# Kernel tuning notes

Hardware: AMD Instinct MI355X
Metric: run time of the kernel (lower is better)

The kernel has to match this reference:

```python
import jax, jax.numpy as jnp
import numpy as np

B, H, S, D = 2, 16, 2048, 64
MASK_NEG = 1e9


def setup_inputs() -> dict:
    key = jax.random.key(0)
    kq, kk, kv, km = jax.random.split(key, 4)
    Q = jax.random.normal(kq, (B, H, S, D), dtype=jnp.float32)
    K = jax.random.normal(kk, (B, H, S, D), dtype=jnp.float32)
    V = jax.random.normal(kv, (B, H, S, D), dtype=jnp.float32)
    # float 0/1 mask, broadcast over heads; 1 = masked-out position
    attn_mask = jax.random.randint(km, (B, 1, S, S), 0, 2).astype(jnp.float32)
    return {"Q": Q, "K": K, "V": V, "attn_mask": attn_mask}


def reference(Q, K, V, attn_mask):
    # scores: [B, H, S, S]
    attn_score = jnp.einsum('bhqd,bhkd->bhqk', Q, K)
    scale = jnp.sqrt(jnp.asarray(K.shape[-1], dtype=jnp.float32))
    attn_scale = attn_score / scale - MASK_NEG * attn_mask
    attn_prob = jax.nn.softmax(attn_scale, axis=-1)
    attn_out = jnp.einsum('bhqk,bhkd->bhqd', attn_prob, V)
    return attn_out
```

## Files before the change

kernel.cpp:

```cpp
#include <hip/hip_runtime.h>


#define S_LEN 2048
#define D_DIM 64
#define WPR   32
#define NIT   32

typedef __attribute__((ext_vector_type(8)))  short bf16x8;
typedef __attribute__((ext_vector_type(4)))  float f32x4;
typedef __attribute__((ext_vector_type(16))) float f32x16;
typedef unsigned long long ull;

__device__ __forceinline__ f32x16 mfma32(bf16x8 a, bf16x8 b, f32x16 c) {
  return __builtin_amdgcn_mfma_f32_32x32x16_bf16(a, b, c, 0, 0, 0);
}
__device__ __forceinline__ f32x4 mfma16(bf16x8 a, bf16x8 b, f32x4 c) {
  return __builtin_amdgcn_mfma_f32_16x16x32_bf16(a, b, c, 0, 0, 0);
}
__device__ __forceinline__ unsigned short f2bf(float f) {
  unsigned u = __builtin_bit_cast(unsigned, f);
  unsigned r = u + 0x7FFFu + ((u >> 16) & 1u);
  return (unsigned short)(r >> 16);
}
__device__ __forceinline__ float bf2f(unsigned short s) {
  unsigned u = ((unsigned)s) << 16;
  return __builtin_bit_cast(float, u);
}
__device__ __forceinline__ unsigned packbf(float a, float b) {
#if __has_builtin(__builtin_amdgcn_cvt_pk_bf16_f32)
  typedef __bf16 bfv2 __attribute__((ext_vector_type(2)));
  bfv2 v = __builtin_amdgcn_cvt_pk_bf16_f32(a, b);
  return __builtin_bit_cast(unsigned, v);
#else
  unsigned ua = __builtin_bit_cast(unsigned, a);
  unsigned ub = __builtin_bit_cast(unsigned, b);
  ua = ua + 0x7FFFu + ((ua >> 16) & 1u);
  ub = ub + 0x7FFFu + ((ub >> 16) & 1u);
  return (ua >> 16) | (ub & 0xFFFF0000u);
#endif
}
__device__ __forceinline__ float fexp2(float x) {
#if __has_builtin(__builtin_amdgcn_exp2f)
  return __builtin_amdgcn_exp2f(x);
#else
  return exp2f(x);
#endif
}
__device__ __forceinline__ bool detect_bf16(const void* maskp) {
  const unsigned short* s = (const unsigned short*)maskp;
  unsigned short v = s[2 * (threadIdx.x & 63)];
  return __ballot(v == (unsigned short)0x3F80) != 0ull;
}
__device__ __forceinline__ int4 cvt_f8(const float* p) {
  float4 f0 = *(const float4*)p;
  float4 f1 = *(const float4*)(p + 4);
  int4 r;
  r.x = (int)packbf(f0.x, f0.y);
  r.y = (int)packbf(f0.z, f0.w);
  r.z = (int)packbf(f1.x, f1.y);
  r.w = (int)packbf(f1.z, f1.w);
  return r;
}

#define C1 0.18033688011112042f
#define C2 1.4426950408889634e9f

__global__ __launch_bounds__(256) void prep_all(
    const void* __restrict__ M, const void* __restrict__ Kin,
    const void* __restrict__ Vin, const void* __restrict__ Qin,
    ull* __restrict__ bits, unsigned short* __restrict__ Kf,
    unsigned short* __restrict__ Vf, unsigned short* __restrict__ Qc) {
  __shared__ __align__(16) unsigned short T[64 * 72];
  const bool isb = detect_bf16(M);
  const unsigned bx = blockIdx.x;
  const int tid = threadIdx.x;

  if (bx < 32768u) {
    unsigned idx = bx * 256u + tid;
    bool on = isb ? (bf2f(((const unsigned short*)M)[idx]) > 0.5f)
                  : (((const float*)M)[idx] > 0.5f);
    ull bm = __ballot(on);
    if ((tid & 63) == 0) {
      unsigned c = idx & 2047u, r = (idx >> 11) & 2047u, bb = idx >> 22;
      bits[(((size_t)(bb * WPR + (c >> 6))) << 11) + r] = bm;
    }
  } else if (bx < 32768u + 2048u) {
    unsigned g = (bx - 32768u) * 256u + tid;
    unsigned lane = g & 63u, f = (g >> 6) & 7u, it = (g >> 9) & 31u, bh = g >> 14;
    unsigned t = f >> 2, dc = f & 3, hi = lane >> 5, l31 = lane & 31;
    size_t src = (size_t)bh * (S_LEN * D_DIM) +
                 (size_t)(it * 64 + t * 32 + l31) * D_DIM + dc * 16 + hi * 8;
    int4 out;
    if (isb) out = *(const int4*)((const unsigned short*)Kin + src);
    else     out = cvt_f8((const float*)Kin + src);
    *(int4*)&Kf[(size_t)g * 8] = out;
  } else if (bx < 32768u + 2048u + 1024u) {
    unsigned idx = bx - (32768u + 2048u);
    unsigned bh = idx >> 5, it = idx & 31u;
    {
      int k = tid >> 2, d0 = (tid & 3) * 16;
      size_t src = (size_t)bh * (S_LEN * D_DIM) + (size_t)(it * 64 + k) * D_DIM + d0;
      int4 a, c;
      if (isb) {
        const unsigned short* s = (const unsigned short*)Vin + src;
        a = *(const int4*)s; c = *(const int4*)(s + 8);
      } else {
        const float* s = (const float*)Vin + src;
        a = cvt_f8(s); c = cvt_f8(s + 8);
      }
      *(int4*)&T[k * 72 + d0] = a;
      *(int4*)&T[k * 72 + d0 + 8] = c;
    }
    __syncthreads();
    #pragma unroll
    for (int h = 0; h < 2; ++h) {
      int c = tid + h * 256;
      int lane = c & 63, f = c >> 6;
      int t = f >> 2, kc = (f >> 1) & 1, dt = f & 1;
      int hi = lane >> 5, l31 = lane & 31;
      unsigned short v[8];
      #pragma unroll
      for (int j = 0; j < 8; ++j)
        v[j] = T[(t * 32 + kc * 16 + hi * 8 + j) * 72 + dt * 32 + l31];
      *(int4*)&Vf[(((size_t)(bh * 32 + it)) * 8 + f) * 512 + lane * 8] = *(int4*)v;
    }
  } else {
    size_t i0 = ((size_t)(bx - (32768u + 2048u + 1024u)) * 256 + tid) * 8;
    unsigned short v[8];
    if (isb) {
      *(int4*)v = *(const int4*)((const unsigned short*)Qin + i0);
      #pragma unroll
      for (int j = 0; j < 8; ++j) v[j] = f2bf(bf2f(v[j]) * C1);
    } else {
      const float* f = (const float*)Qin + i0;
      #pragma unroll
      for (int j = 0; j < 4; ++j)
        *((unsigned*)v + j) = packbf(f[2 * j] * C1, f[2 * j + 1] * C1);
    }
    *(int4*)&Qc[i0] = *(int4*)v;
  }
}

__global__ __launch_bounds__(256, 4) void attn_fast(
    const unsigned short* __restrict__ Qc, const unsigned short* __restrict__ Kf,
    const unsigned short* __restrict__ Vf, const ull* __restrict__ bits,
    const void* __restrict__ maskp, void* __restrict__ Op) {
  __shared__ float Comb[2][32][64];
  __shared__ float Lc[4][32];

  const bool isb = detect_bf16(maskp);
  const int tid  = threadIdx.x;
  const int wave = tid >> 6;
  const int lane = tid & 63;
  const int hi   = lane >> 5;
  const int l31  = lane & 31;
  const int id   = blockIdx.x;
  const int slot = id >> 3;
  const int bh   = (id & 7) * 4 + (slot & 3);
  const int q0   = (slot >> 2) * 32;
  const int b    = bh >> 4;
  const size_t base = (size_t)bh * S_LEN * D_DIM;
  const int xidx = ((lane ^ 32) & 63) * 4;

  bf16x8 qf[4];
  #pragma unroll
  for (int dc = 0; dc < 4; ++dc)
    qf[dc] = *(const bf16x8*)&Qc[base + (size_t)(q0 + l31) * D_DIM + dc * 16 + hi * 8];

  f32x16 acc_o[2];
  float lsum = 0.f;
  #pragma unroll
  for (int r = 0; r < 16; ++r) { acc_o[0][r] = 0.f; acc_o[1][r] = 0.f; }

  for (int i = 0; i < NIT / 4; ++i) {
    const int it = wave * (NIT / 4) + i;
    const size_t fb = ((size_t)(bh * 32 + it)) * 8 * 512;

    ull w = bits[(((size_t)(b * WPR + it)) << 11) + q0 + l31] >> (hi * 4);
    unsigned wt[2] = {(unsigned)w, (unsigned)(w >> 32)};

    #pragma unroll
    for (int t = 0; t < 2; ++t) {
      const unsigned short* Kb = Kf + fb + (size_t)(t * 4) * 512 + lane * 8;
      f32x16 sc;
      #pragma unroll
      for (int r = 0; r < 16; ++r) sc[r] = 0.f;
      #pragma unroll
      for (int dc = 0; dc < 4; ++dc) {
        bf16x8 kfr = *(const bf16x8*)(Kb + dc * 512);
        sc = mfma32(kfr, qf[dc], sc);
      }

      float p[16];
      #pragma unroll
      for (int r = 0; r < 16; ++r) {
        float e = fexp2(sc[r]);
        unsigned bit = (wt[t] >> ((r & 3) + 8 * (r >> 2))) & 1u;
        p[r] = bit ? 0.0f : e;
        lsum += p[r];
      }

      #pragma unroll
      for (int kc = 0; kc < 2; ++kc) {
        unsigned pk0 = packbf(p[8 * kc + 0], p[8 * kc + 1]);
        unsigned pk1 = packbf(p[8 * kc + 2], p[8 * kc + 3]);
        unsigned pk2 = packbf(p[8 * kc + 4], p[8 * kc + 5]);
        unsigned pk3 = packbf(p[8 * kc + 6], p[8 * kc + 7]);
        unsigned x0 = (unsigned)__builtin_amdgcn_ds_bpermute(xidx, (int)pk0);
        unsigned x1 = (unsigned)__builtin_amdgcn_ds_bpermute(xidx, (int)pk1);
        unsigned x2 = (unsigned)__builtin_amdgcn_ds_bpermute(xidx, (int)pk2);
        unsigned x3 = (unsigned)__builtin_amdgcn_ds_bpermute(xidx, (int)pk3);
        uint4 d;
        d.x = hi ? x2 : pk0;
        d.y = hi ? x3 : pk1;
        d.z = hi ? pk2 : x0;
        d.w = hi ? pk3 : x1;
        bf16x8 pf = __builtin_bit_cast(bf16x8, d);

        const unsigned short* Vb = Vf + fb + (size_t)(t * 4 + kc * 2) * 512 + lane * 8;
        #pragma unroll
        for (int dt = 0; dt < 2; ++dt) {
          bf16x8 vfr = *(const bf16x8*)(Vb + dt * 512);
          acc_o[dt] = mfma32(pf, vfr, acc_o[dt]);
        }
      }
    }
  }

  {
    int li = __builtin_bit_cast(int, lsum);
    float other = __builtin_bit_cast(float, __builtin_amdgcn_ds_bpermute(xidx, li));
    lsum += other;
  }

  __syncthreads();
  if (wave >= 2) {
    #pragma unroll
    for (int dt = 0; dt < 2; ++dt)
      #pragma unroll
      for (int r = 0; r < 16; ++r)
        Comb[wave - 2][dt * 16 + r][lane] = acc_o[dt][r];
  }
  if (hi == 0) Lc[wave][l31] = lsum;
  __syncthreads();
  if (wave < 2) {
    #pragma unroll
    for (int dt = 0; dt < 2; ++dt)
      #pragma unroll
      for (int r = 0; r < 16; ++r)
        acc_o[dt][r] += Comb[wave][dt * 16 + r][lane];
  }
  __syncthreads();
  if (wave == 1) {
    #pragma unroll
    for (int dt = 0; dt < 2; ++dt)
      #pragma unroll
      for (int r = 0; r < 16; ++r)
        Comb[0][dt * 16 + r][lane] = acc_o[dt][r];
  }
  __syncthreads();
  if (wave == 0) {
    #pragma unroll
    for (int r = 0; r < 16; ++r) {
      int m = (r & 3) + 8 * (r >> 2) + 4 * hi;
      float o0 = acc_o[0][r] + Comb[0][r][lane];
      float o1 = acc_o[1][r] + Comb[0][16 + r][lane];
      float lv = Lc[0][m] + Lc[1][m] + Lc[2][m] + Lc[3][m];
      float inv = 1.0f / lv;
      size_t idx = base + (size_t)(q0 + m) * D_DIM + l31;
      if (isb) {
        ((unsigned short*)Op)[idx]      = f2bf(o0 * inv);
        ((unsigned short*)Op)[idx + 32] = f2bf(o1 * inv);
      } else {
        ((float*)Op)[idx]      = o0 * inv;
        ((float*)Op)[idx + 32] = o1 * inv;
      }
    }
  }
}

__global__ __launch_bounds__(256, 2) void attn_fallback(
    const void* __restrict__ Qp, const void* __restrict__ Kp,
    const void* __restrict__ Vp, const void* __restrict__ maskp,
    void* __restrict__ Op) {
  __shared__ __align__(16) short QKlds[128 * 72];
  __shared__ __align__(16) short Vtlds[64 * 72];
  __shared__ __align__(16) short Plds2[128 * 72];

  const bool isb = detect_bf16(maskp);
  const int tid  = threadIdx.x;
  const int wave = tid >> 6;
  const int lane = tid & 63;
  const int l15  = lane & 15;
  const int quad = lane >> 4;
  const int q0   = blockIdx.x * 128;
  const int bh   = blockIdx.y;
  const int b    = bh >> 4;
  const size_t base = (size_t)bh * S_LEN * D_DIM;

  const short* Qs = (const short*)Qp; const float* Qf = (const float*)Qp;
  const short* Ks = (const short*)Kp; const float* Kf2 = (const float*)Kp;
  const short* Vs = (const short*)Vp; const float* Vf2 = (const float*)Vp;

  if (isb) {
    const short* Qg = Qs + base + (size_t)q0 * D_DIM;
    #pragma unroll
    for (int p = 0; p < 4; ++p) {
      int e = p * 2048 + tid * 8;
      *(int4*)&QKlds[(e >> 6) * 72 + (e & 63)] = *(const int4*)(Qg + e);
    }
  } else {
    const float* Qg = Qf + base + (size_t)q0 * D_DIM;
    #pragma unroll
    for (int p = 0; p < 4; ++p) {
      int e = p * 2048 + tid * 8;
      *(int4*)&QKlds[(e >> 6) * 72 + (e & 63)] = cvt_f8(Qg + e);
    }
  }
  __syncthreads();
  bf16x8 qf[2][2];
  #pragma unroll
  for (int mi = 0; mi < 2; ++mi)
    #pragma unroll
    for (int kt = 0; kt < 2; ++kt)
      qf[mi][kt] = *(const bf16x8*)&QKlds[(wave * 32 + mi * 16 + l15) * 72 + kt * 32 + quad * 8];
  __syncthreads();

  f32x4 acc_o[2][4];
  f32x4 acc_l[2];
  const f32x4 zero4 = {0.f, 0.f, 0.f, 0.f};
  #pragma unroll
  for (int mi = 0; mi < 2; ++mi) {
    acc_l[mi] = zero4;
    #pragma unroll
    for (int nt = 0; nt < 4; ++nt) acc_o[mi][nt] = zero4;
  }
  bf16x8 onesB;
  {
    short ov = (l15 == 0) ? (short)0x3F80 : (short)0;
    #pragma unroll
    for (int i = 0; i < 8; ++i) onesB[i] = ov;
  }

  for (int it = 0; it < NIT; ++it) {
    const int k0 = it * 64;
    if (isb) {
      const short* Kg = Ks + base + (size_t)k0 * D_DIM;
      #pragma unroll
      for (int p = 0; p < 2; ++p) {
        int e = p * 2048 + tid * 8;
        *(int4*)&QKlds[(e >> 6) * 72 + (e & 63)] = *(const int4*)(Kg + e);
      }
    } else {
      const float* Kg = Kf2 + base + (size_t)k0 * D_DIM;
      #pragma unroll
      for (int p = 0; p < 2; ++p) {
        int e = p * 2048 + tid * 8;
        *(int4*)&QKlds[(e >> 6) * 72 + (e & 63)] = cvt_f8(Kg + e);
      }
    }
    {
      const int r0 = (tid >> 3) * 2;
      const int d0 = (tid & 7) * 8;
      unsigned short as_[8], bs_[8];
      if (isb) {
        const short* Vg = Vs + base + (size_t)k0 * D_DIM;
        *(int4*)as_ = *(const int4*)(Vg + r0 * D_DIM + d0);
        *(int4*)bs_ = *(const int4*)(Vg + (r0 + 1) * D_DIM + d0);
      } else {
        const float* Vg = Vf2 + base + (size_t)k0 * D_DIM;
        *(int4*)as_ = cvt_f8(Vg + r0 * D_DIM + d0);
        *(int4*)bs_ = cvt_f8(Vg + (r0 + 1) * D_DIM + d0);
      }
      #pragma unroll
      for (int j = 0; j < 8; ++j) {
        int d = d0 + j;
        int blk = (r0 >> 3) ^ (d >> 3);
        unsigned pk = (unsigned)as_[j] | ((unsigned)bs_[j] << 16);
        *(unsigned*)&Vtlds[d * 72 + blk * 8 + (r0 & 7)] = pk;
      }
    }
    __syncthreads();

    f32x4 sc[2][4];
    #pragma unroll
    for (int mi = 0; mi < 2; ++mi)
      #pragma unroll
      for (int nt = 0; nt < 4; ++nt) sc[mi][nt] = zero4;
    #pragma unroll
    for (int nt = 0; nt < 4; ++nt) {
      bf16x8 kf0 = *(const bf16x8*)&QKlds[(nt * 16 + l15) * 72 + quad * 8];
      bf16x8 kf1 = *(const bf16x8*)&QKlds[(nt * 16 + l15) * 72 + 32 + quad * 8];
      #pragma unroll
      for (int mi = 0; mi < 2; ++mi) {
        sc[mi][nt] = mfma16(qf[mi][0], kf0, sc[mi][nt]);
        sc[mi][nt] = mfma16(qf[mi][1], kf1, sc[mi][nt]);
      }
    }

    #pragma unroll
    for (int mi = 0; mi < 2; ++mi) {
      #pragma unroll
      for (int nt = 0; nt < 4; ++nt) {
        #pragma unroll
        for (int reg = 0; reg < 4; ++reg) {
          int rg = q0 + wave * 32 + mi * 16 + quad * 4 + reg;
          size_t mix = (size_t)b * S_LEN * S_LEN + (size_t)rg * S_LEN + k0 + nt * 16 + l15;
          float mv = isb ? bf2f(((const unsigned short*)maskp)[mix])
                         : ((const float*)maskp)[mix];
          float y = sc[mi][nt][reg] * C1 - mv * C2;
          Plds2[(wave * 32 + mi * 16 + quad * 4 + reg) * 72 + nt * 16 + l15] =
              (short)f2bf(fexp2(y));
        }
      }
    }
    __syncthreads();

    #pragma unroll
    for (int kt = 0; kt < 2; ++kt) {
      bf16x8 pf[2];
      #pragma unroll
      for (int mi = 0; mi < 2; ++mi)
        pf[mi] = *(const bf16x8*)&Plds2[(wave * 32 + mi * 16 + l15) * 72 + kt * 32 + quad * 8];
      #pragma unroll
      for (int nt = 0; nt < 4; ++nt) {
        int d = nt * 16 + l15;
        int kb = (kt * 4 + quad) ^ (d >> 3);
        bf16x8 vf = *(const bf16x8*)&Vtlds[d * 72 + kb * 8];
        #pragma unroll
        for (int mi = 0; mi < 2; ++mi)
          acc_o[mi][nt] = mfma16(pf[mi], vf, acc_o[mi][nt]);
      }
      #pragma unroll
      for (int mi = 0; mi < 2; ++mi)
        acc_l[mi] = mfma16(pf[mi], onesB, acc_l[mi]);
    }
    __syncthreads();
  }

  #pragma unroll
  for (int mi = 0; mi < 2; ++mi) {
    #pragma unroll
    for (int reg = 0; reg < 4; ++reg) {
      float lv = __shfl(acc_l[mi][reg], lane & 48, 64);
      float inv = 1.0f / lv;
      #pragma unroll
      for (int nt = 0; nt < 4; ++nt) {
        float o = acc_o[mi][nt][reg] * inv;
        size_t idx = base + (size_t)(q0 + wave * 32 + mi * 16 + quad * 4 + reg) * D_DIM + nt * 16 + l15;
        if (isb) ((unsigned short*)Op)[idx] = f2bf(o);
        else     ((float*)Op)[idx] = o;
      }
    }
  }
}

extern "C" void kernel_launch(void* const* d_in, const int* in_sizes, int n_in,
                              void* d_out, int out_size, void* d_ws, size_t ws_size,
                              hipStream_t stream) {
  const void* Q = d_in[0];
  const void* K = d_in[1];
  const void* V = d_in[2];
  const void* M = d_in[3];

  dim3 block(256);
  const size_t bits_bytes = (size_t)2 * S_LEN * S_LEN / 8;
  const size_t tens_bytes = (size_t)2 * 16 * S_LEN * D_DIM * 2;

  if (ws_size >= bits_bytes + 3 * tens_bytes) {
    char* ws = (char*)d_ws;
    ull* bits = (ull*)ws;
    unsigned short* Kf = (unsigned short*)(ws + bits_bytes);
    unsigned short* Vf = (unsigned short*)(ws + bits_bytes + tens_bytes);
    unsigned short* Qc = (unsigned short*)(ws + bits_bytes + 2 * tens_bytes);
    prep_all<<<dim3(32768 + 2048 + 1024 + 2048), block, 0, stream>>>(
        M, K, V, Q, bits, Kf, Vf, Qc);
    attn_fast<<<dim3(2048), block, 0, stream>>>(Qc, Kf, Vf, bits, M, d_out);
  } else {
    attn_fallback<<<dim3(S_LEN / 128, 32), block, 0, stream>>>(Q, K, V, M, d_out);
  }
}
```

Measured before the change: 187.1 us.

## Permute K rows and mask bits to drop P-fragment lane swaps; row sums via MFMA

The K fragment rows and the mask bitmask are permuted in the prep kernel, so the score MFMA output layout matches the A-operand layout of the PV MFMA. This removes the four ds_bpermute cross-lane swaps per P fragment. The row-sum accumulation is moved from scalar adds to an extra MFMA against a ones vector, with a new store pattern for the partial sums. The cost is one extra MFMA per PV step, 16 more accumulator registers and more complex index bookkeeping.

```diff
diff --git a/kernel.cpp b/kernel.cpp
--- a/kernel.cpp
+++ b/kernel.cpp
@@ -26,17 +26,14 @@
   unsigned u = ((unsigned)s) << 16;
   return __builtin_bit_cast(float, u);
 }
+typedef __bf16 bfv2 __attribute__((ext_vector_type(2)));
 __device__ __forceinline__ unsigned packbf(float a, float b) {
 #if __has_builtin(__builtin_amdgcn_cvt_pk_bf16_f32)
-  typedef __bf16 bfv2 __attribute__((ext_vector_type(2)));
   bfv2 v = __builtin_amdgcn_cvt_pk_bf16_f32(a, b);
   return __builtin_bit_cast(unsigned, v);
 #else
-  unsigned ua = __builtin_bit_cast(unsigned, a);
-  unsigned ub = __builtin_bit_cast(unsigned, b);
-  ua = ua + 0x7FFFu + ((ua >> 16) & 1u);
-  ub = ub + 0x7FFFu + ((ub >> 16) & 1u);
-  return (ua >> 16) | (ub & 0xFFFF0000u);
+  bfv2 v = {(__bf16)a, (__bf16)b};
+  return __builtin_bit_cast(unsigned, v);
 #endif
 }
 __device__ __forceinline__ float fexp2(float x) {
@@ -65,6 +62,11 @@
 #define C1 0.18033688011112042f
 #define C2 1.4426950408889634e9f
 
+__device__ __forceinline__ unsigned permrow(unsigned x) {
+  unsigned m12 = x & 12u;
+  return (m12 == 4u) ? x + 4u : (m12 == 8u) ? x - 4u : x;
+}
+
 __global__ __launch_bounds__(256) void prep_all(
     const void* __restrict__ M, const void* __restrict__ Kin,
     const void* __restrict__ Vin, const void* __restrict__ Qin,
@@ -81,6 +83,8 @@
                   : (((const float*)M)[idx] > 0.5f);
     ull bm = __ballot(on);
     if ((tid & 63) == 0) {
+      const ull M1 = 0x00F000F000F000F0ULL, M2 = 0x0F000F000F000F00ULL;
+      bm = (bm & ~(M1 | M2)) | ((bm & M1) << 4) | ((bm & M2) >> 4);
       unsigned c = idx & 2047u, r = (idx >> 11) & 2047u, bb = idx >> 22;
       bits[(((size_t)(bb * WPR + (c >> 6))) << 11) + r] = bm;
     }
@@ -89,7 +93,7 @@
     unsigned lane = g & 63u, f = (g >> 6) & 7u, it = (g >> 9) & 31u, bh = g >> 14;
     unsigned t = f >> 2, dc = f & 3, hi = lane >> 5, l31 = lane & 31;
     size_t src = (size_t)bh * (S_LEN * D_DIM) +
-                 (size_t)(it * 64 + t * 32 + l31) * D_DIM + dc * 16 + hi * 8;
+                 (size_t)(it * 64 + t * 32 + permrow(l31)) * D_DIM + dc * 16 + hi * 8;
     int4 out;
     if (isb) out = *(const int4*)((const unsigned short*)Kin + src);
     else     out = cvt_f8((const float*)Kin + src);
@@ -160,7 +164,6 @@
   const int q0   = (slot >> 2) * 32;
   const int b    = bh >> 4;
   const size_t base = (size_t)bh * S_LEN * D_DIM;
-  const int xidx = ((lane ^ 32) & 63) * 4;
 
   bf16x8 qf[4];
   #pragma unroll
@@ -168,9 +171,16 @@
     qf[dc] = *(const bf16x8*)&Qc[base + (size_t)(q0 + l31) * D_DIM + dc * 16 + hi * 8];
 
   f32x16 acc_o[2];
-  float lsum = 0.f;
+  f32x16 acc_l;
   #pragma unroll
-  for (int r = 0; r < 16; ++r) { acc_o[0][r] = 0.f; acc_o[1][r] = 0.f; }
+  for (int r = 0; r < 16; ++r) { acc_o[0][r] = 0.f; acc_o[1][r] = 0.f; acc_l[r] = 0.f; }
+
+  bf16x8 onesB;
+  {
+    short ov = (l31 == 0) ? (short)0x3F80 : (short)0;
+    #pragma unroll
+    for (int i = 0; i < 8; ++i) onesB[i] = ov;
+  }
 
   for (int i = 0; i < NIT / 4; ++i) {
     const int it = wave * (NIT / 4) + i;
@@ -197,24 +207,15 @@
         float e = fexp2(sc[r]);
         unsigned bit = (wt[t] >> ((r & 3) + 8 * (r >> 2))) & 1u;
         p[r] = bit ? 0.0f : e;
-        lsum += p[r];
       }
 
       #pragma unroll
       for (int kc = 0; kc < 2; ++kc) {
-        unsigned pk0 = packbf(p[8 * kc + 0], p[8 * kc + 1]);
-        unsigned pk1 = packbf(p[8 * kc + 2], p[8 * kc + 3]);
-        unsigned pk2 = packbf(p[8 * kc + 4], p[8 * kc + 5]);
-        unsigned pk3 = packbf(p[8 * kc + 6], p[8 * kc + 7]);
-        unsigned x0 = (unsigned)__builtin_amdgcn_ds_bpermute(xidx, (int)pk0);
-        unsigned x1 = (unsigned)__builtin_amdgcn_ds_bpermute(xidx, (int)pk1);
-        unsigned x2 = (unsigned)__builtin_amdgcn_ds_bpermute(xidx, (int)pk2);
-        unsigned x3 = (unsigned)__builtin_amdgcn_ds_bpermute(xidx, (int)pk3);
         uint4 d;
-        d.x = hi ? x2 : pk0;
-        d.y = hi ? x3 : pk1;
-        d.z = hi ? pk2 : x0;
-        d.w = hi ? pk3 : x1;
+        d.x = packbf(p[8 * kc + 0], p[8 * kc + 1]);
+        d.y = packbf(p[8 * kc + 2], p[8 * kc + 3]);
+        d.z = packbf(p[8 * kc + 4], p[8 * kc + 5]);
+        d.w = packbf(p[8 * kc + 6], p[8 * kc + 7]);
         bf16x8 pf = __builtin_bit_cast(bf16x8, d);
 
         const unsigned short* Vb = Vf + fb + (size_t)(t * 4 + kc * 2) * 512 + lane * 8;
@@ -223,14 +224,9 @@
           bf16x8 vfr = *(const bf16x8*)(Vb + dt * 512);
           acc_o[dt] = mfma32(pf, vfr, acc_o[dt]);
         }
-      }
-    }
-  }
-
-  {
-    int li = __builtin_bit_cast(int, lsum);
-    float other = __builtin_bit_cast(float, __builtin_amdgcn_ds_bpermute(xidx, li));
-    lsum += other;
+        acc_l = mfma32(pf, onesB, acc_l);
+      }
+    }
   }
 
   __syncthreads();
@@ -241,7 +237,11 @@
       for (int r = 0; r < 16; ++r)
         Comb[wave - 2][dt * 16 + r][lane] = acc_o[dt][r];
   }
-  if (hi == 0) Lc[wave][l31] = lsum;
+  if (l31 == 0) {
+    #pragma unroll
+    for (int r = 0; r < 16; ++r)
+      Lc[wave][(r & 3) + 8 * (r >> 2) + 4 * hi] = acc_l[r];
+  }
   __syncthreads();
   if (wave < 2) {
     #pragma unroll
```

Measured after the change: 194.0 us. 1.04x slower.

## Permute K rows and mask bits to drop bpermute exchange; prefetch K/V fragments

Applied to the files above, without the earlier changes.

The prep kernel now permutes K rows within each 32-row tile (swapping row groups 4-7 and 8-11) and applies the matching nibble swap to the packed mask bits. With that layout the P fragment produced by the QK^T MFMA can feed the PV MFMA directly, so the four ds_bpermute exchanges and selects per chunk are removed. The main loop also loads all K and V fragments for an iteration up front, before the mask word and the compute, to hide global load latency. This uses more registers and relies on the row permutation matching the MFMA output layout exactly.

```diff
diff --git a/kernel.cpp b/kernel.cpp
--- a/kernel.cpp
+++ b/kernel.cpp
@@ -65,6 +65,11 @@
 #define C1 0.18033688011112042f
 #define C2 1.4426950408889634e9f
 
+__device__ __forceinline__ unsigned permrow(unsigned x) {
+  unsigned m12 = x & 12u;
+  return (m12 == 4u) ? x + 4u : (m12 == 8u) ? x - 4u : x;
+}
+
 __global__ __launch_bounds__(256) void prep_all(
     const void* __restrict__ M, const void* __restrict__ Kin,
     const void* __restrict__ Vin, const void* __restrict__ Qin,
@@ -81,6 +86,8 @@
                   : (((const float*)M)[idx] > 0.5f);
     ull bm = __ballot(on);
     if ((tid & 63) == 0) {
+      const ull M1 = 0x00F000F000F000F0ULL, M2 = 0x0F000F000F000F00ULL;
+      bm = (bm & ~(M1 | M2)) | ((bm & M1) << 4) | ((bm & M2) >> 4);
       unsigned c = idx & 2047u, r = (idx >> 11) & 2047u, bb = idx >> 22;
       bits[(((size_t)(bb * WPR + (c >> 6))) << 11) + r] = bm;
     }
@@ -89,7 +96,7 @@
     unsigned lane = g & 63u, f = (g >> 6) & 7u, it = (g >> 9) & 31u, bh = g >> 14;
     unsigned t = f >> 2, dc = f & 3, hi = lane >> 5, l31 = lane & 31;
     size_t src = (size_t)bh * (S_LEN * D_DIM) +
-                 (size_t)(it * 64 + t * 32 + l31) * D_DIM + dc * 16 + hi * 8;
+                 (size_t)(it * 64 + t * 32 + permrow(l31)) * D_DIM + dc * 16 + hi * 8;
     int4 out;
     if (isb) out = *(const int4*)((const unsigned short*)Kin + src);
     else     out = cvt_f8((const float*)Kin + src);
@@ -175,21 +182,31 @@
   for (int i = 0; i < NIT / 4; ++i) {
     const int it = wave * (NIT / 4) + i;
     const size_t fb = ((size_t)(bh * 32 + it)) * 8 * 512;
-
+    const unsigned short* Fb = Kf + fb + lane * 8;
+    const unsigned short* Vb = Vf + fb + lane * 8;
+
+    bf16x8 kfr[2][4], vfr[2][4];
+    #pragma unroll
+    for (int t = 0; t < 2; ++t)
+      #pragma unroll
+      for (int dc = 0; dc < 4; ++dc)
+        kfr[t][dc] = *(const bf16x8*)(Fb + (size_t)(t * 4 + dc) * 512);
+    #pragma unroll
+    for (int t = 0; t < 2; ++t)
+      #pragma unroll
+      for (int f = 0; f < 4; ++f)
+        vfr[t][f] = *(const bf16x8*)(Vb + (size_t)(t * 4 + f) * 512);
     ull w = bits[(((size_t)(b * WPR + it)) << 11) + q0 + l31] >> (hi * 4);
     unsigned wt[2] = {(unsigned)w, (unsigned)(w >> 32)};
 
     #pragma unroll
     for (int t = 0; t < 2; ++t) {
-      const unsigned short* Kb = Kf + fb + (size_t)(t * 4) * 512 + lane * 8;
       f32x16 sc;
       #pragma unroll
       for (int r = 0; r < 16; ++r) sc[r] = 0.f;
       #pragma unroll
-      for (int dc = 0; dc < 4; ++dc) {
-        bf16x8 kfr = *(const bf16x8*)(Kb + dc * 512);
-        sc = mfma32(kfr, qf[dc], sc);
-      }
+      for (int dc = 0; dc < 4; ++dc)
+        sc = mfma32(kfr[t][dc], qf[dc], sc);
 
       float p[16];
       #pragma unroll
@@ -202,27 +219,15 @@
 
       #pragma unroll
       for (int kc = 0; kc < 2; ++kc) {
-        unsigned pk0 = packbf(p[8 * kc + 0], p[8 * kc + 1]);
-        unsigned pk1 = packbf(p[8 * kc + 2], p[8 * kc + 3]);
-        unsigned pk2 = packbf(p[8 * kc + 4], p[8 * kc + 5]);
-        unsigned pk3 = packbf(p[8 * kc + 6], p[8 * kc + 7]);
-        unsigned x0 = (unsigned)__builtin_amdgcn_ds_bpermute(xidx, (int)pk0);
-        unsigned x1 = (unsigned)__builtin_amdgcn_ds_bpermute(xidx, (int)pk1);
-        unsigned x2 = (unsigned)__builtin_amdgcn_ds_bpermute(xidx, (int)pk2);
-        unsigned x3 = (unsigned)__builtin_amdgcn_ds_bpermute(xidx, (int)pk3);
         uint4 d;
-        d.x = hi ? x2 : pk0;
-        d.y = hi ? x3 : pk1;
-        d.z = hi ? pk2 : x0;
-        d.w = hi ? pk3 : x1;
+        d.x = packbf(p[8 * kc + 0], p[8 * kc + 1]);
+        d.y = packbf(p[8 * kc + 2], p[8 * kc + 3]);
+        d.z = packbf(p[8 * kc + 4], p[8 * kc + 5]);
+        d.w = packbf(p[8 * kc + 6], p[8 * kc + 7]);
         bf16x8 pf = __builtin_bit_cast(bf16x8, d);
-
-        const unsigned short* Vb = Vf + fb + (size_t)(t * 4 + kc * 2) * 512 + lane * 8;
         #pragma unroll
-        for (int dt = 0; dt < 2; ++dt) {
-          bf16x8 vfr = *(const bf16x8*)(Vb + dt * 512);
-          acc_o[dt] = mfma32(pf, vfr, acc_o[dt]);
-        }
+        for (int dt = 0; dt < 2; ++dt)
+          acc_o[dt] = mfma32(pf, vfr[t][kc * 2 + dt], acc_o[dt]);
       }
     }
   }
```

Measured after the change: 189.8 us. No clear change (+1.5%).
